# Performance work log

Hardware: AMD Instinct MI355X
Metric: run time of the kernel (lower is better)

## Reference

```python
import jax, jax.numpy as jnp
import numpy as np

B, T, E = 2, 2048, 2048
H, D = 16, 128
KVH = H // 2
THETA = 10000.0

def make_rope(dim, seq_len, theta):
    inv_freqs = 1.0 / (theta ** (jnp.arange(0, dim, 2, dtype=jnp.float32) / dim))
    positions = jnp.arange(seq_len, dtype=jnp.float32)
    freqs = positions[:, None] * inv_freqs[None, :]  # (T, D/2)
    return jax.lax.complex(jnp.cos(freqs), jnp.sin(freqs))

def apply_rope(x, rope):
    # x: (B, h, T, D), rope: (T, D/2) complex
    xr = x.astype(jnp.float32).reshape(*x.shape[:-1], -1, 2)
    xc = jax.lax.complex(xr[..., 0], xr[..., 1])
    out = xc * rope[None, None, :, :]
    return jnp.stack([jnp.real(out), jnp.imag(out)], axis=-1).reshape(x.shape).astype(x.dtype)

def setup_inputs() -> dict:
    key = jax.random.key(0)
    ks = jax.random.split(key, 5)
    x = jax.random.normal(ks[0], (B, T, E), dtype=jnp.float32)
    mask = jnp.tril(jnp.ones((T, T), dtype=jnp.int32))[None, None]  # causal (1,1,T,T)
    s = 0.02
    wq = jax.random.normal(ks[1], (E, H * D), dtype=jnp.float32) * s
    wk = jax.random.normal(ks[2], (E, KVH * D), dtype=jnp.float32) * s
    wv = jax.random.normal(ks[3], (E, KVH * D), dtype=jnp.float32) * s
    wo = jax.random.normal(ks[4], (H * D, E), dtype=jnp.float32) * s
    return {"x": x, "mask": mask, "wq": wq, "wk": wk, "wv": wv, "wo": wo}

def reference(x, mask, wq, wk, wv, wo):
    rope = make_rope(D, T, THETA)
    q = (x @ wq).reshape(B, T, H, D).transpose(0, 2, 1, 3)      # (B,H,T,D)
    k = (x @ wk).reshape(B, T, KVH, D).transpose(0, 2, 1, 3)    # (B,KVH,T,D)
    v = (x @ wv).reshape(B, T, KVH, D).transpose(0, 2, 1, 3)
    q = apply_rope(q, rope)
    k = apply_rope(k, rope)
    # GQA: repeat kv heads to match query heads
    k = jnp.repeat(k, H // KVH, axis=1)
    v = jnp.repeat(v, H // KVH, axis=1)
    scale = D ** -0.5
    attn = jnp.einsum('bhqd,bhkd->bhqk', q, k) * scale
    attn = jnp.where(mask == 0, -jnp.inf, attn)
    attn = jax.nn.softmax(attn, axis=-1)
    attn = jnp.where(jnp.isnan(attn), 0.0, attn)
    out = jnp.einsum('bhqk,bhkd->bhqd', attn, v)
    out = out.transpose(0, 2, 1, 3).reshape(B, T, H * D)
    return out @ wo
```

## Files before the change

### kernel.cpp

```cpp
#include <hip/hip_runtime.h>
#include <math.h>

#define Bb   2
#define Tt   2048
#define Ee   2048
#define Hh   16
#define KVHh 8
#define Dd   128
#define Mm   (Bb*Tt)

typedef unsigned short u16;
typedef __bf16 bf16x8 __attribute__((ext_vector_type(8)));
typedef float  f32x4  __attribute__((ext_vector_type(4)));

__device__ __forceinline__ u16 f2b(float f) {
    union { float f; unsigned u; } v; v.f = f;
    unsigned r = v.u + 0x7fffu + ((v.u >> 16) & 1u);
    return (u16)(r >> 16);
}
__device__ __forceinline__ u16 f2b_fast(float f) {
    union { float f; unsigned u; } v; v.f = f;
    return (u16)((v.u + 0x8000u) >> 16);
}
__device__ __forceinline__ float b2f(u16 h) {
    union { float f; unsigned u; } v; v.u = ((unsigned)h) << 16;
    return v.f;
}

__device__ __forceinline__ void gl_lds16(const u16* g, u16* l) {
    __builtin_amdgcn_global_load_lds(
        (const __attribute__((address_space(1))) void*)g,
        (__attribute__((address_space(3))) void*)l,
        16, 0, 0);
}

__global__ void cast_x_kernel(const float* __restrict__ x, u16* __restrict__ xb, int n4) {
    int i = blockIdx.x * blockDim.x + threadIdx.x;
    if (i >= n4) return;
    float4 f = ((const float4*)x)[i];
    unsigned lo = (unsigned)f2b(f.x) | ((unsigned)f2b(f.y) << 16);
    unsigned hi = (unsigned)f2b(f.z) | ((unsigned)f2b(f.w) << 16);
    ((uint2*)xb)[i] = make_uint2(lo, hi);
}

__global__ void addf4_kernel(float* __restrict__ o, const float* __restrict__ a, int n4) {
    int i = blockIdx.x * blockDim.x + threadIdx.x;
    if (i >= n4) return;
    float4 x = ((const float4*)o)[i];
    float4 y = ((const float4*)a)[i];
    x.x += y.x; x.y += y.y; x.z += y.z; x.w += y.w;
    ((float4*)o)[i] = x;
}

__global__ void transpose_cast4_kernel(const float* __restrict__ wq, const float* __restrict__ wk,
                                       const float* __restrict__ wv, const float* __restrict__ wo,
                                       u16* __restrict__ btqkv, u16* __restrict__ bto) {
    __shared__ float tile[32][33];
    int job = blockIdx.z;
    const float* W; u16* Bt; int C;
    if (job == 0)      { W = wq; Bt = btqkv;                      C = 2048; }
    else if (job == 1) { W = wk; Bt = btqkv + (size_t)2048 * Ee;  C = 1024; }
    else if (job == 2) { W = wv; Bt = btqkv + (size_t)3072 * Ee;  C = 1024; }
    else               { W = wo; Bt = bto;                        C = 2048; }
    int c0 = blockIdx.x * 32, r0 = blockIdx.y * 32;
    if (c0 >= C) return;
    int x = threadIdx.x, y = threadIdx.y;
    for (int j = y; j < 32; j += 8)
        tile[j][x] = W[(size_t)(r0 + j) * C + c0 + x];
    __syncthreads();
    for (int j = y; j < 32; j += 8)
        Bt[(size_t)(c0 + j) * 2048 + r0 + x] = f2b(tile[x][j]);
}

__global__ void transpose_v_kernel(const u16* __restrict__ v, u16* __restrict__ vt) {
    __shared__ u16 tile[32][34];
    int x = threadIdx.x, y = threadIdx.y;
    int c0 = blockIdx.x * 32;
    int r0 = blockIdx.y * 32;
    int bk = blockIdx.z;
    for (int j = y; j < 32; j += 8)
        tile[j][x] = v[((size_t)bk * Tt + r0 + j) * Dd + c0 + x];
    __syncthreads();
    for (int j = y; j < 32; j += 8)
        vt[((size_t)bk * Dd + c0 + j) * Tt + r0 + x] = tile[x][j];
}

__global__ void rope_kernel(u16* __restrict__ q, u16* __restrict__ k) {
    const int QP = Bb * Hh * Tt * (Dd / 2);
    const int KP = Bb * KVHh * Tt * (Dd / 2);
    int idx = blockIdx.x * blockDim.x + threadIdx.x;
    if (idx >= QP + KP) return;
    u16* ptr; int p;
    if (idx < QP) { ptr = q; p = idx; } else { ptr = k; p = idx - QP; }
    int d2 = p & 63;
    int row = p >> 6;
    int t = row & (Tt - 1);
    float ex = (float)(2 * d2) * (1.0f / 128.0f);
    float inv = expf(-ex * 9.210340371976184f);
    float fr = (float)t * inv;
    float c = cosf(fr), s = sinf(fr);
    size_t e0 = (size_t)row * Dd + 2 * d2;
    unsigned pair = *(const unsigned*)(ptr + e0);
    float x0 = b2f((u16)(pair & 0xffff));
    float x1 = b2f((u16)(pair >> 16));
    float o0 = x0 * c - x1 * s;
    float o1 = x0 * s + x1 * c;
    *(unsigned*)(ptr + e0) = (unsigned)f2b(o0) | ((unsigned)f2b(o1) << 16);
}

__global__ __launch_bounds__(512, 2) void gemm8_kernel(
    const u16* __restrict__ A0, const u16* __restrict__ Bt0,
    int Ndim, int Kdim, int Kstride, int mode,
    u16* __restrict__ qo, u16* __restrict__ ko, u16* __restrict__ vo,
    float* __restrict__ fo, float* __restrict__ fo2)
{
    __shared__ u16 sm[2][2][256 * 64];
    const int tid = threadIdx.x;
    const int lane = tid & 63, w = tid >> 6;
    const int quad = lane >> 4, l15 = lane & 15;
    const int bn = blockIdx.x, bm = blockIdx.y, kz = blockIdx.z;
    const u16* A  = A0  + (size_t)kz * Kdim;
    const u16* Bt = Bt0 + (size_t)kz * Kdim;
    const int wm = (w >> 2) * 128, wn = (w & 3) * 64;
    const int rowA0 = bm * 256, rowB0 = bn * 256;

    const int srow = lane >> 3;
    const int scolsw = (((lane & 7) ^ srow) << 3);
    const int wa = w & 3, wb = w >> 2;
    const int cAlo = (wm >> 3) + 2 * wa;
    const int cAhi = (wm >> 3) + 8 + 2 * wa;
    const int cBlo = (wn >> 3) + 2 * wb;
    const int cBhi = (wn >> 3) + 4 + 2 * wb;

    const int col0 = ((quad ^ (l15 & 7)) << 3);
    const int col1 = (((4 | quad) ^ (l15 & 7)) << 3);

    f32x4 acc[8][4];
#pragma unroll
    for (int i = 0; i < 8; i++)
#pragma unroll
        for (int j = 0; j < 4; j++) acc[i][j] = (f32x4){0.f, 0.f, 0.f, 0.f};

#define STAGE_PAIR(G, Grow0, ldsb, cb, kk) do { \
    gl_lds16((G) + (size_t)((Grow0) + (cb) * 8 + srow) * Kstride + (kk) + scolsw, \
             (ldsb) + (cb) * 512); \
    gl_lds16((G) + (size_t)((Grow0) + (cb) * 8 + 8 + srow) * Kstride + (kk) + scolsw, \
             (ldsb) + (cb) * 512 + 512); \
} while (0)

    STAGE_PAIR(A,  rowA0, &sm[0][0][0], cAlo, 0);
    STAGE_PAIR(Bt, rowB0, &sm[0][1][0], cBlo, 0);
    STAGE_PAIR(Bt, rowB0, &sm[0][1][0], cBhi, 0);
    STAGE_PAIR(A,  rowA0, &sm[0][0][0], cAhi, 0);
    asm volatile("s_waitcnt vmcnt(4)" ::: "memory");
    __builtin_amdgcn_s_barrier();
    __builtin_amdgcn_sched_barrier(0);

    bf16x8 a4[4][2], bA[2][2], bB[2][2];
    const int NT = Kdim >> 6;

    for (int t = 0; t < NT; ++t) {
        u16* As = &sm[t & 1][0][0];
        u16* Bs = &sm[t & 1][1][0];
        u16* An = &sm[(t + 1) & 1][0][0];
        u16* Bn = &sm[(t + 1) & 1][1][0];
        const int kk = (t + 1) << 6;
        const bool st = (t + 1 < NT);

#pragma unroll
        for (int i = 0; i < 4; i++) {
            const u16* p = As + (wm + i * 16 + l15) * 64;
            a4[i][0] = *(const bf16x8*)(p + col0);
            a4[i][1] = *(const bf16x8*)(p + col1);
        }
#pragma unroll
        for (int j = 0; j < 2; j++) {
            const u16* p = Bs + (wn + j * 16 + l15) * 64;
            bA[j][0] = *(const bf16x8*)(p + col0);
            bA[j][1] = *(const bf16x8*)(p + col1);
        }
        if (st) STAGE_PAIR(A, rowA0, An, cAlo, kk);
        __builtin_amdgcn_sched_barrier(0);
        __builtin_amdgcn_s_barrier();
        __builtin_amdgcn_sched_barrier(0);
        __builtin_amdgcn_s_setprio(1);
#pragma unroll
        for (int kc = 0; kc < 2; kc++)
#pragma unroll
            for (int i = 0; i < 4; i++)
#pragma unroll
                for (int j = 0; j < 2; j++)
                    acc[i][j] = __builtin_amdgcn_mfma_f32_16x16x32_bf16(a4[i][kc], bA[j][kc], acc[i][j], 0, 0, 0);
        __builtin_amdgcn_s_setprio(0);
        __builtin_amdgcn_sched_barrier(0);
        if (st) { asm volatile("s_waitcnt vmcnt(4)" ::: "memory"); }
        else    { asm volatile("s_waitcnt vmcnt(2)" ::: "memory"); }
        __builtin_amdgcn_s_barrier();
        __builtin_amdgcn_sched_barrier(0);

#pragma unroll
        for (int j = 0; j < 2; j++) {
            const u16* p = Bs + (wn + 32 + j * 16 + l15) * 64;
            bB[j][0] = *(const bf16x8*)(p + col0);
            bB[j][1] = *(const bf16x8*)(p + col1);
        }
        if (st) STAGE_PAIR(Bt, rowB0, Bn, cBlo, kk);
        __builtin_amdgcn_sched_barrier(0);
        __builtin_amdgcn_s_barrier();
        __builtin_amdgcn_sched_barrier(0);
        __builtin_amdgcn_s_setprio(1);
#pragma unroll
        for (int kc = 0; kc < 2; kc++)
#pragma unroll
            for (int i = 0; i < 4; i++)
#pragma unroll
                for (int j = 0; j < 2; j++)
                    acc[i][j + 2] = __builtin_amdgcn_mfma_f32_16x16x32_bf16(a4[i][kc], bB[j][kc], acc[i][j + 2], 0, 0, 0);
        __builtin_amdgcn_s_setprio(0);
        __builtin_amdgcn_sched_barrier(0);
        if (st) { asm volatile("s_waitcnt vmcnt(4)" ::: "memory"); }
        else    { asm volatile("s_waitcnt vmcnt(0)" ::: "memory"); }
        __builtin_amdgcn_s_barrier();
        __builtin_amdgcn_sched_barrier(0);

#pragma unroll
        for (int i = 0; i < 4; i++) {
            const u16* p = As + (wm + 64 + i * 16 + l15) * 64;
            a4[i][0] = *(const bf16x8*)(p + col0);
            a4[i][1] = *(const bf16x8*)(p + col1);
        }
        if (st) STAGE_PAIR(Bt, rowB0, Bn, cBhi, kk);
        __builtin_amdgcn_sched_barrier(0);
        __builtin_amdgcn_s_barrier();
        __builtin_amdgcn_sched_barrier(0);
        __builtin_amdgcn_s_setprio(1);
#pragma unroll
        for (int kc = 0; kc < 2; kc++)
#pragma unroll
            for (int i = 0; i < 4; i++)
#pragma unroll
                for (int j = 0; j < 2; j++)
                    acc[i + 4][j] = __builtin_amdgcn_mfma_f32_16x16x32_bf16(a4[i][kc], bA[j][kc], acc[i + 4][j], 0, 0, 0);
        __builtin_amdgcn_s_setprio(0);
        __builtin_amdgcn_sched_barrier(0);
        if (st) { asm volatile("s_waitcnt vmcnt(4)" ::: "memory"); }
        __builtin_amdgcn_s_barrier();
        __builtin_amdgcn_sched_barrier(0);

        if (st) STAGE_PAIR(A, rowA0, An, cAhi, kk);
        __builtin_amdgcn_sched_barrier(0);
        __builtin_amdgcn_s_barrier();
        __builtin_amdgcn_sched_barrier(0);
        __builtin_amdgcn_s_setprio(1);
#pragma unroll
        for (int kc = 0; kc < 2; kc++)
#pragma unroll
            for (int i = 0; i < 4; i++)
#pragma unroll
                for (int j = 0; j < 2; j++)
                    acc[i + 4][j + 2] = __builtin_amdgcn_mfma_f32_16x16x32_bf16(a4[i][kc], bB[j][kc], acc[i + 4][j + 2], 0, 0, 0);
        __builtin_amdgcn_s_setprio(0);
        __builtin_amdgcn_sched_barrier(0);
        if (st) { asm volatile("s_waitcnt vmcnt(4)" ::: "memory"); }
        __builtin_amdgcn_s_barrier();
        __builtin_amdgcn_sched_barrier(0);
    }
#undef STAGE_PAIR

    float* ft = kz ? fo2 : fo;
#pragma unroll
    for (int i = 0; i < 8; i++)
#pragma unroll
        for (int j = 0; j < 4; j++)
#pragma unroll
            for (int r = 0; r < 4; r++) {
                int m = rowA0 + wm + i * 16 + quad * 4 + r;
                int n = rowB0 + wn + j * 16 + l15;
                float val = acc[i][j][r];
                if (mode == 0) {
                    int b = m >> 11, tq = m & (Tt - 1);
                    if (n < 2048) {
                        int h = n >> 7, d = n & 127;
                        qo[(((size_t)(b * Hh + h)) * Tt + tq) * Dd + d] = f2b(val);
                    } else if (n < 3072) {
                        int h = (n - 2048) >> 7, d = n & 127;
                        ko[(((size_t)(b * KVHh + h)) * Tt + tq) * Dd + d] = f2b(val);
                    } else {
                        int h = (n - 3072) >> 7, d = n & 127;
                        vo[(((size_t)(b * KVHh + h)) * Tt + tq) * Dd + d] = f2b(val);
                    }
                } else {
                    ft[(size_t)m * Ndim + n] = val;
                }
            }
}

#define LDKV 136
#define LDVT 72
#define LDP  72
#define GRPU (64*LDKV + 128*LDVT + 128*LDP)

__global__ __launch_bounds__(512) void flash_kernel(
    const u16* __restrict__ q, const u16* __restrict__ k, const u16* __restrict__ vt,
    u16* __restrict__ attn)
{
    __shared__ u16 S[2 * GRPU];

    int tid = threadIdx.x;
    int grp = tid >> 8;
    int gtid = tid & 255;
    int lane = tid & 63, w4 = gtid >> 6;
    int quad = lane >> 4, l15 = lane & 15;
    int pr = blockIdx.x;
    int bh = blockIdx.y;
    int b = bh >> 4, h = bh & 15;
    int kvh = h >> 1;
    const u16* qbase = q + (size_t)bh * Tt * Dd;
    const u16* kbase = k + ((size_t)(b * KVHh + kvh)) * Tt * Dd;
    const u16* vtbase = vt + ((size_t)(b * KVHh + kvh)) * Dd * Tt;

    u16* Ksh  = S + grp * GRPU;
    u16* Vtsh = Ksh + 64 * LDKV;
    u16* Psh  = Vtsh + 128 * LDVT;
    u16* P0 = Psh + (2 * w4) * 16 * LDP;
    u16* P1 = Psh + (2 * w4 + 1) * 16 * LDP;
    u16* KA = S;
    u16* VA = S + 64 * LDKV;

    const float sc2 = 0.08838834764831845f * 1.4426950408889634f;
    const int qt_h = 15 - pr;
    const int light_nkt = 2 * (pr + 1);

    const int krow = gtid >> 4, kcol = (gtid & 15) * 8;
    const int vrow = gtid >> 3, vcol = (gtid & 7) * 8;

    int qt = grp ? pr : qt_h;
    int row0 = qt * 128 + w4 * 32;

    bf16x8 qf0[4], qf1[4];
#define LOAD_QF() do { \
    const u16* qr0 = qbase + (size_t)(row0 + l15) * Dd + quad * 8; \
    const u16* qr1 = qbase + (size_t)(row0 + 16 + l15) * Dd + quad * 8; \
    _Pragma("unroll") \
    for (int c = 0; c < 4; c++) { \
        qf0[c] = *(const bf16x8*)(qr0 + c * 32); \
        qf1[c] = *(const bf16x8*)(qr1 + c * 32); \
    } \
} while (0)
    LOAD_QF();

    f32x4 o0[8], o1[8];
#pragma unroll
    for (int i = 0; i < 8; i++) { o0[i] = (f32x4){0.f,0.f,0.f,0.f}; o1[i] = (f32x4){0.f,0.f,0.f,0.f}; }
    float l0[4] = {0.f,0.f,0.f,0.f}, l1[4] = {0.f,0.f,0.f,0.f};

    for (int it = 0; it < 17; it++) {
        if (grp == 1 && it == light_nkt) {
            float linv0[4], linv1[4];
#pragma unroll
            for (int r = 0; r < 4; r++) {
                float a = l0[r];
                a += __shfl_xor(a, 1); a += __shfl_xor(a, 2);
                a += __shfl_xor(a, 4); a += __shfl_xor(a, 8);
                linv0[r] = 1.0f / a;
                float c2 = l1[r];
                c2 += __shfl_xor(c2, 1); c2 += __shfl_xor(c2, 2);
                c2 += __shfl_xor(c2, 4); c2 += __shfl_xor(c2, 8);
                linv1[r] = 1.0f / c2;
            }
#pragma unroll
            for (int di = 0; di < 8; di++)
#pragma unroll
                for (int r = 0; r < 4; r++) {
                    int ta = row0 + quad * 4 + r;
                    int tb = row0 + 16 + quad * 4 + r;
                    size_t ma = (size_t)b * Tt + ta;
                    size_t mb = (size_t)b * Tt + tb;
                    attn[ma * (Hh * Dd) + h * Dd + di * 16 + l15] = f2b(o0[di][r] * linv0[r]);
                    attn[mb * (Hh * Dd) + h * Dd + di * 16 + l15] = f2b(o1[di][r] * linv1[r]);
                }
#pragma unroll
            for (int i = 0; i < 8; i++) { o0[i] = (f32x4){0.f,0.f,0.f,0.f}; o1[i] = (f32x4){0.f,0.f,0.f,0.f}; }
#pragma unroll
            for (int r = 0; r < 4; r++) { l0[r] = 0.f; l1[r] = 0.f; }
            qt = qt_h; row0 = qt * 128 + w4 * 32;
            LOAD_QF();
        }
        const int kt = (grp == 0) ? it : (it < light_nkt ? it : 17 + (it - light_nkt));
        const bool shareA = (grp == 1) && (it < light_nkt);
        const u16* Kr = shareA ? KA : Ksh;
        const u16* Vr = shareA ? VA : Vtsh;

        if (!shareA) {
#pragma unroll
            for (int j = 0; j < 4; j++) {
                int chunk = j * 256 + gtid;
                int rk = chunk >> 4, ck = chunk & 15;
                uint4 dk = *(const uint4*)(kbase + (size_t)(kt * 64 + rk) * Dd + ck * 8);
                *(uint4*)(Ksh + rk * LDKV + ck * 8) = dk;
                int rv = chunk >> 3, cv = chunk & 7;
                uint4 dv = *(const uint4*)(vtbase + (size_t)rv * Tt + kt * 64 + cv * 8);
                *(uint4*)(Vtsh + rv * LDVT + cv * 8) = dv;
            }
        }
        __syncthreads();

        bool skip = (kt * 64) > (row0 + 31);
        if (!skip) {
            f32x4 s0[4], s1[4];
#pragma unroll
            for (int ni = 0; ni < 4; ni++) { s0[ni] = (f32x4){0.f,0.f,0.f,0.f}; s1[ni] = (f32x4){0.f,0.f,0.f,0.f}; }
#pragma unroll
            for (int c = 0; c < 4; c++)
#pragma unroll
                for (int ni = 0; ni < 4; ni++) {
                    bf16x8 kf = *(const bf16x8*)(Kr + (ni * 16 + l15) * LDKV + c * 32 + quad * 8);
                    s0[ni] = __builtin_amdgcn_mfma_f32_16x16x32_bf16(qf0[c], kf, s0[ni], 0, 0, 0);
                    s1[ni] = __builtin_amdgcn_mfma_f32_16x16x32_bf16(qf1[c], kf, s1[ni], 0, 0, 0);
                }

            if (kt * 64 + 63 > row0) {
#pragma unroll
                for (int ni = 0; ni < 4; ni++)
#pragma unroll
                    for (int r = 0; r < 4; r++) {
                        int kcolm = kt * 64 + ni * 16 + l15;
                        int qa = row0 + quad * 4 + r;
                        int qb2 = row0 + 16 + quad * 4 + r;
                        if (kcolm > qa)  s0[ni][r] = -__builtin_inff();
                        if (kcolm > qb2) s1[ni][r] = -__builtin_inff();
                    }
            }

#pragma unroll
            for (int ni = 0; ni < 4; ni++)
#pragma unroll
                for (int r = 0; r < 4; r++) {
                    float p0 = exp2f(s0[ni][r] * sc2);
                    l0[r] += p0;
                    P0[(quad * 4 + r) * LDP + ni * 16 + l15] = f2b_fast(p0);
                    float p1 = exp2f(s1[ni][r] * sc2);
                    l1[r] += p1;
                    P1[(quad * 4 + r) * LDP + ni * 16 + l15] = f2b_fast(p1);
                }
        }
        __syncthreads();

        if (!skip) {
#pragma unroll
            for (int c = 0; c < 2; c++) {
                bf16x8 pf0 = *(const bf16x8*)(P0 + l15 * LDP + c * 32 + quad * 8);
                bf16x8 pf1 = *(const bf16x8*)(P1 + l15 * LDP + c * 32 + quad * 8);
#pragma unroll
                for (int di = 0; di < 8; di++) {
                    bf16x8 vf = *(const bf16x8*)(Vr + (di * 16 + l15) * LDVT + c * 32 + quad * 8);
                    o0[di] = __builtin_amdgcn_mfma_f32_16x16x32_bf16(pf0, vf, o0[di], 0, 0, 0);
                    o1[di] = __builtin_amdgcn_mfma_f32_16x16x32_bf16(pf1, vf, o1[di], 0, 0, 0);
                }
            }
        }
        __syncthreads();
    }

    float* Obuf = (float*)S;
    float* Lbuf = (float*)((char*)S + 128 * 132 * 4);
    if (grp == 1) {
        float ls0[4], ls1[4];
#pragma unroll
        for (int r = 0; r < 4; r++) {
            float a = l0[r];
            a += __shfl_xor(a, 1); a += __shfl_xor(a, 2);
            a += __shfl_xor(a, 4); a += __shfl_xor(a, 8);
            ls0[r] = a;
            float c2 = l1[r];
            c2 += __shfl_xor(c2, 1); c2 += __shfl_xor(c2, 2);
            c2 += __shfl_xor(c2, 4); c2 += __shfl_xor(c2, 8);
            ls1[r] = c2;
        }
#pragma unroll
        for (int di = 0; di < 8; di++)
#pragma unroll
            for (int r = 0; r < 4; r++) {
                Obuf[(w4 * 32 + quad * 4 + r) * 132 + di * 16 + l15] = o0[di][r];
                Obuf[(w4 * 32 + 16 + quad * 4 + r) * 132 + di * 16 + l15] = o1[di][r];
            }
        if (l15 == 0)
#pragma unroll
            for (int r = 0; r < 4; r++) {
                Lbuf[w4 * 32 + quad * 4 + r] = ls0[r];
                Lbuf[w4 * 32 + 16 + quad * 4 + r] = ls1[r];
            }
    }
    __syncthreads();
    if (grp == 0) {
        float linv0[4], linv1[4];
#pragma unroll
        for (int r = 0; r < 4; r++) {
            float a = l0[r];
            a += __shfl_xor(a, 1); a += __shfl_xor(a, 2);
            a += __shfl_xor(a, 4); a += __shfl_xor(a, 8);
            linv0[r] = 1.0f / (a + Lbuf[w4 * 32 + quad * 4 + r]);
            float c2 = l1[r];
            c2 += __shfl_xor(c2, 1); c2 += __shfl_xor(c2, 2);
            c2 += __shfl_xor(c2, 4); c2 += __shfl_xor(c2, 8);
            linv1[r] = 1.0f / (c2 + Lbuf[w4 * 32 + 16 + quad * 4 + r]);
        }
#pragma unroll
        for (int di = 0; di < 8; di++)
#pragma unroll
            for (int r = 0; r < 4; r++) {
                float v0 = o0[di][r] + Obuf[(w4 * 32 + quad * 4 + r) * 132 + di * 16 + l15];
                float v1 = o1[di][r] + Obuf[(w4 * 32 + 16 + quad * 4 + r) * 132 + di * 16 + l15];
                int ta = row0 + quad * 4 + r;
                int tb = row0 + 16 + quad * 4 + r;
                size_t ma = (size_t)b * Tt + ta;
                size_t mb = (size_t)b * Tt + tb;
                attn[ma * (Hh * Dd) + h * Dd + di * 16 + l15] = f2b(v0 * linv0[r]);
                attn[mb * (Hh * Dd) + h * Dd + di * 16 + l15] = f2b(v1 * linv1[r]);
            }
    }
#undef LOAD_QF
}

extern "C" void kernel_launch(void* const* d_in, const int* in_sizes, int n_in,
                              void* d_out, int out_size, void* d_ws, size_t ws_size,
                              hipStream_t stream) {
    const float* x  = (const float*)d_in[0];
    const float* wq = (const float*)d_in[2];
    const float* wk = (const float*)d_in[3];
    const float* wv = (const float*)d_in[4];
    const float* wo = (const float*)d_in[5];
    float* out = (float*)d_out;

    char* ws = (char*)d_ws;
    u16* xb    = (u16*)ws; ws += (size_t)Mm * Ee * 2;
    u16* btqkv = (u16*)ws; ws += (size_t)4096 * Ee * 2;
    u16* bto   = (u16*)ws; ws += (size_t)Ee * (Hh * Dd) * 2;
    u16* qb    = (u16*)ws; ws += (size_t)Bb * Hh * Tt * Dd * 2;
    u16* kb    = (u16*)ws; ws += (size_t)Bb * KVHh * Tt * Dd * 2;
    u16* vb    = (u16*)ws; ws += (size_t)Bb * KVHh * Tt * Dd * 2;
    u16* vtb   = (u16*)ws; ws += (size_t)Bb * KVHh * Dd * Tt * 2;
    u16* attn  = (u16*)ws; ws += (size_t)Mm * (Hh * Dd) * 2;

    float* fo2 = (float*)qb;

    cast_x_kernel<<<(Mm * Ee / 4 + 255) / 256, 256, 0, stream>>>(x, xb, Mm * Ee / 4);

    transpose_cast4_kernel<<<dim3(64, 64, 4), dim3(32, 8), 0, stream>>>(wq, wk, wv, wo, btqkv, bto);

    gemm8_kernel<<<dim3(16, 16, 1), 512, 0, stream>>>(xb, btqkv, 4096, Ee, Ee, 0,
                                                      qb, kb, vb, nullptr, nullptr);

    {
        int total = Bb * Hh * Tt * 64 + Bb * KVHh * Tt * 64;
        rope_kernel<<<(total + 255) / 256, 256, 0, stream>>>(qb, kb);
    }

    transpose_v_kernel<<<dim3(Dd / 32, Tt / 32, Bb * KVHh), dim3(32, 8), 0, stream>>>(vb, vtb);

    flash_kernel<<<dim3(Tt / 256, Bb * Hh), 512, 0, stream>>>(qb, kb, vtb, attn);

    gemm8_kernel<<<dim3(8, 16, 2), 512, 0, stream>>>(attn, bto, 2048, (Hh * Dd) / 2, Hh * Dd, 1,
                                                     nullptr, nullptr, nullptr, out, fo2);
    addf4_kernel<<<(Mm * Ee / 4 + 255) / 256, 256, 0, stream>>>(out, fo2, Mm * Ee / 4);
}
```

Before: 361.9 us.

## Restructure GEMM LDS pipeline with split A registers and early B prefetch

The GEMM main loop now keeps separate register sets for the low and high A halves. It loads the B fragments for the next iteration ahead of the last MFMA block, and merges the first two compute phases so one barrier round is removed. The vmcnt waits are tightened to match the new staging order. In the attention kernel, a __syncthreads between writing the P tile and the PV MFMA is removed, which relies on each wave reading only the P rows it wrote itself. The aim is fewer barriers and better overlap of LDS reads with MFMA, at the cost of more registers and possible LDS race hazards.

New measurement: 358.7 us. Within noise of the previous version (-0.9%).

```diff
diff --git a/kernel.cpp b/kernel.cpp
--- a/kernel.cpp
+++ b/kernel.cpp
@@ -152,12 +152,19 @@
     STAGE_PAIR(Bt, rowB0, &sm[0][1][0], cBlo, 0);
     STAGE_PAIR(Bt, rowB0, &sm[0][1][0], cBhi, 0);
     STAGE_PAIR(A,  rowA0, &sm[0][0][0], cAhi, 0);
-    asm volatile("s_waitcnt vmcnt(4)" ::: "memory");
+    asm volatile("s_waitcnt vmcnt(2)" ::: "memory");
     __builtin_amdgcn_s_barrier();
     __builtin_amdgcn_sched_barrier(0);
 
-    bf16x8 a4[4][2], bA[2][2], bB[2][2];
+    bf16x8 a4lo[4][2], a4hi[4][2], bA[2][2], bB[2][2];
     const int NT = Kdim >> 6;
+
+#pragma unroll
+    for (int j = 0; j < 2; j++) {
+        const u16* p = &sm[0][1][0] + (wn + j * 16 + l15) * 64;
+        bA[j][0] = *(const bf16x8*)(p + col0);
+        bA[j][1] = *(const bf16x8*)(p + col1);
+    }
 
     for (int t = 0; t < NT; ++t) {
         u16* As = &sm[t & 1][0][0];
@@ -170,40 +177,35 @@
 #pragma unroll
         for (int i = 0; i < 4; i++) {
             const u16* p = As + (wm + i * 16 + l15) * 64;
-            a4[i][0] = *(const bf16x8*)(p + col0);
-            a4[i][1] = *(const bf16x8*)(p + col1);
-        }
-#pragma unroll
-        for (int j = 0; j < 2; j++) {
-            const u16* p = Bs + (wn + j * 16 + l15) * 64;
-            bA[j][0] = *(const bf16x8*)(p + col0);
-            bA[j][1] = *(const bf16x8*)(p + col1);
+            a4lo[i][0] = *(const bf16x8*)(p + col0);
+            a4lo[i][1] = *(const bf16x8*)(p + col1);
         }
         if (st) STAGE_PAIR(A, rowA0, An, cAlo, kk);
         __builtin_amdgcn_sched_barrier(0);
         __builtin_amdgcn_s_barrier();
         __builtin_amdgcn_sched_barrier(0);
-        __builtin_amdgcn_s_setprio(1);
-#pragma unroll
-        for (int kc = 0; kc < 2; kc++)
-#pragma unroll
-            for (int i = 0; i < 4; i++)
-#pragma unroll
-                for (int j = 0; j < 2; j++)
-                    acc[i][j] = __builtin_amdgcn_mfma_f32_16x16x32_bf16(a4[i][kc], bA[j][kc], acc[i][j], 0, 0, 0);
-        __builtin_amdgcn_s_setprio(0);
-        __builtin_amdgcn_sched_barrier(0);
-        if (st) { asm volatile("s_waitcnt vmcnt(4)" ::: "memory"); }
-        else    { asm volatile("s_waitcnt vmcnt(2)" ::: "memory"); }
-        __builtin_amdgcn_s_barrier();
-        __builtin_amdgcn_sched_barrier(0);
-
 #pragma unroll
         for (int j = 0; j < 2; j++) {
             const u16* p = Bs + (wn + 32 + j * 16 + l15) * 64;
             bB[j][0] = *(const bf16x8*)(p + col0);
             bB[j][1] = *(const bf16x8*)(p + col1);
         }
+        __builtin_amdgcn_sched_barrier(0);
+        __builtin_amdgcn_s_setprio(1);
+#pragma unroll
+        for (int kc = 0; kc < 2; kc++)
+#pragma unroll
+            for (int i = 0; i < 4; i++)
+#pragma unroll
+                for (int j = 0; j < 2; j++)
+                    acc[i][j] = __builtin_amdgcn_mfma_f32_16x16x32_bf16(a4lo[i][kc], bA[j][kc], acc[i][j], 0, 0, 0);
+        __builtin_amdgcn_s_setprio(0);
+        __builtin_amdgcn_sched_barrier(0);
+        if (st) { asm volatile("s_waitcnt vmcnt(2)" ::: "memory"); }
+        else    { asm volatile("s_waitcnt vmcnt(0)" ::: "memory"); }
+        __builtin_amdgcn_s_barrier();
+        __builtin_amdgcn_sched_barrier(0);
+
         if (st) STAGE_PAIR(Bt, rowB0, Bn, cBlo, kk);
         __builtin_amdgcn_sched_barrier(0);
         __builtin_amdgcn_s_barrier();
@@ -215,19 +217,18 @@
             for (int i = 0; i < 4; i++)
 #pragma unroll
                 for (int j = 0; j < 2; j++)
-                    acc[i][j + 2] = __builtin_amdgcn_mfma_f32_16x16x32_bf16(a4[i][kc], bB[j][kc], acc[i][j + 2], 0, 0, 0);
+                    acc[i][j + 2] = __builtin_amdgcn_mfma_f32_16x16x32_bf16(a4lo[i][kc], bB[j][kc], acc[i][j + 2], 0, 0, 0);
         __builtin_amdgcn_s_setprio(0);
         __builtin_amdgcn_sched_barrier(0);
-        if (st) { asm volatile("s_waitcnt vmcnt(4)" ::: "memory"); }
-        else    { asm volatile("s_waitcnt vmcnt(0)" ::: "memory"); }
+        if (st) { asm volatile("s_waitcnt vmcnt(2)" ::: "memory"); }
         __builtin_amdgcn_s_barrier();
         __builtin_amdgcn_sched_barrier(0);
 
 #pragma unroll
         for (int i = 0; i < 4; i++) {
             const u16* p = As + (wm + 64 + i * 16 + l15) * 64;
-            a4[i][0] = *(const bf16x8*)(p + col0);
-            a4[i][1] = *(const bf16x8*)(p + col1);
+            a4hi[i][0] = *(const bf16x8*)(p + col0);
+            a4hi[i][1] = *(const bf16x8*)(p + col1);
         }
         if (st) STAGE_PAIR(Bt, rowB0, Bn, cBhi, kk);
         __builtin_amdgcn_sched_barrier(0);
@@ -240,10 +241,10 @@
             for (int i = 0; i < 4; i++)
 #pragma unroll
                 for (int j = 0; j < 2; j++)
-                    acc[i + 4][j] = __builtin_amdgcn_mfma_f32_16x16x32_bf16(a4[i][kc], bA[j][kc], acc[i + 4][j], 0, 0, 0);
+                    acc[i + 4][j] = __builtin_amdgcn_mfma_f32_16x16x32_bf16(a4hi[i][kc], bA[j][kc], acc[i + 4][j], 0, 0, 0);
         __builtin_amdgcn_s_setprio(0);
         __builtin_amdgcn_sched_barrier(0);
-        if (st) { asm volatile("s_waitcnt vmcnt(4)" ::: "memory"); }
+        if (st) { asm volatile("s_waitcnt vmcnt(2)" ::: "memory"); }
         __builtin_amdgcn_s_barrier();
         __builtin_amdgcn_sched_barrier(0);
 
@@ -251,6 +252,15 @@
         __builtin_amdgcn_sched_barrier(0);
         __builtin_amdgcn_s_barrier();
         __builtin_amdgcn_sched_barrier(0);
+        if (st) {
+#pragma unroll
+            for (int j = 0; j < 2; j++) {
+                const u16* p = Bn + (wn + j * 16 + l15) * 64;
+                bA[j][0] = *(const bf16x8*)(p + col0);
+                bA[j][1] = *(const bf16x8*)(p + col1);
+            }
+        }
+        __builtin_amdgcn_sched_barrier(0);
         __builtin_amdgcn_s_setprio(1);
 #pragma unroll
         for (int kc = 0; kc < 2; kc++)
@@ -258,10 +268,10 @@
             for (int i = 0; i < 4; i++)
 #pragma unroll
                 for (int j = 0; j < 2; j++)
-                    acc[i + 4][j + 2] = __builtin_amdgcn_mfma_f32_16x16x32_bf16(a4[i][kc], bB[j][kc], acc[i + 4][j + 2], 0, 0, 0);
+                    acc[i + 4][j + 2] = __builtin_amdgcn_mfma_f32_16x16x32_bf16(a4hi[i][kc], bB[j][kc], acc[i + 4][j + 2], 0, 0, 0);
         __builtin_amdgcn_s_setprio(0);
         __builtin_amdgcn_sched_barrier(0);
-        if (st) { asm volatile("s_waitcnt vmcnt(4)" ::: "memory"); }
+        if (st) { asm volatile("s_waitcnt vmcnt(2)" ::: "memory"); }
         __builtin_amdgcn_s_barrier();
         __builtin_amdgcn_sched_barrier(0);
     }
@@ -443,10 +453,8 @@
                     l1[r] += p1;
                     P1[(quad * 4 + r) * LDP + ni * 16 + l15] = f2b_fast(p1);
                 }
-        }
-        __syncthreads();
-
-        if (!skip) {
+
+
 #pragma unroll
             for (int c = 0; c < 2; c++) {
                 bf16x8 pf0 = *(const bf16x8*)(P0 + l15 * LDP + c * 32 + quad * 8);
```

## Replace split-K output projection with 128x256-tile GEMM and drop add kernel

Applied to the files above, without the earlier changes.

The output projection previously ran as a split-K (2-way) 256x256-tile GEMM writing two fp32 partial buffers, followed by a separate elementwise add kernel. A new GEMM kernel uses 128x256 tiles over the full K, launching 256 blocks directly into the output, which removes the partial-sum write, reread and extra launch. The flash kernel also drops a __syncthreads between writing P to LDS and the PV MFMA, which cuts a barrier but risks a race if P rows are read across waves.

New measurement: 346.2 us. 1.05x faster.

```diff
diff --git a/kernel.cpp b/kernel.cpp
--- a/kernel.cpp
+++ b/kernel.cpp
@@ -41,15 +41,6 @@
     unsigned lo = (unsigned)f2b(f.x) | ((unsigned)f2b(f.y) << 16);
     unsigned hi = (unsigned)f2b(f.z) | ((unsigned)f2b(f.w) << 16);
     ((uint2*)xb)[i] = make_uint2(lo, hi);
-}
-
-__global__ void addf4_kernel(float* __restrict__ o, const float* __restrict__ a, int n4) {
-    int i = blockIdx.x * blockDim.x + threadIdx.x;
-    if (i >= n4) return;
-    float4 x = ((const float4*)o)[i];
-    float4 y = ((const float4*)a)[i];
-    x.x += y.x; x.y += y.y; x.z += y.z; x.w += y.w;
-    ((float4*)o)[i] = x;
 }
 
 __global__ void transpose_cast4_kernel(const float* __restrict__ wq, const float* __restrict__ wk,
@@ -112,15 +103,15 @@
     const u16* __restrict__ A0, const u16* __restrict__ Bt0,
     int Ndim, int Kdim, int Kstride, int mode,
     u16* __restrict__ qo, u16* __restrict__ ko, u16* __restrict__ vo,
-    float* __restrict__ fo, float* __restrict__ fo2)
+    float* __restrict__ fo)
 {
     __shared__ u16 sm[2][2][256 * 64];
     const int tid = threadIdx.x;
     const int lane = tid & 63, w = tid >> 6;
     const int quad = lane >> 4, l15 = lane & 15;
-    const int bn = blockIdx.x, bm = blockIdx.y, kz = blockIdx.z;
-    const u16* A  = A0  + (size_t)kz * Kdim;
-    const u16* Bt = Bt0 + (size_t)kz * Kdim;
+    const int bn = blockIdx.x, bm = blockIdx.y;
+    const u16* A  = A0;
+    const u16* Bt = Bt0;
     const int wm = (w >> 2) * 128, wn = (w & 3) * 64;
     const int rowA0 = bm * 256, rowB0 = bn * 256;
 
@@ -267,7 +258,6 @@
     }
 #undef STAGE_PAIR
 
-    float* ft = kz ? fo2 : fo;
 #pragma unroll
     for (int i = 0; i < 8; i++)
 #pragma unroll
@@ -290,8 +280,166 @@
                         vo[(((size_t)(b * KVHh + h)) * Tt + tq) * Dd + d] = f2b(val);
                     }
                 } else {
-                    ft[(size_t)m * Ndim + n] = val;
+                    fo[(size_t)m * Ndim + n] = val;
                 }
+            }
+}
+
+__global__ __launch_bounds__(512, 2) void gemm8n_kernel(
+    const u16* __restrict__ A, const u16* __restrict__ Bt,
+    int Ndim, int Kdim,
+    float* __restrict__ fo)
+{
+    __shared__ u16 sm[2][384 * 64];
+    const int tid = threadIdx.x;
+    const int lane = tid & 63, w = tid >> 6;
+    const int quad = lane >> 4, l15 = lane & 15;
+    const int bn = blockIdx.x, bm = blockIdx.y;
+    const int wm = (w >> 2) * 64, wn = (w & 3) * 64;
+    const int rowA0 = bm * 128, rowB0 = bn * 256;
+
+    const int srow = lane >> 3;
+    const int scolsw = (((lane & 7) ^ srow) << 3);
+    const int cA = 2 * w;
+    const int cBlo = ((w & 3) * 8) + 2 * (w >> 2);
+    const int cBhi = cBlo + 4;
+
+    const int col0 = ((quad ^ (l15 & 7)) << 3);
+    const int col1 = (((4 | quad) ^ (l15 & 7)) << 3);
+
+    f32x4 acc[4][4];
+#pragma unroll
+    for (int i = 0; i < 4; i++)
+#pragma unroll
+        for (int j = 0; j < 4; j++) acc[i][j] = (f32x4){0.f, 0.f, 0.f, 0.f};
+
+#define STAGE_PAIR(G, Grow0, ldsb, cb, kk) do { \
+    gl_lds16((G) + (size_t)((Grow0) + (cb) * 8 + srow) * Kdim + (kk) + scolsw, \
+             (ldsb) + (cb) * 512); \
+    gl_lds16((G) + (size_t)((Grow0) + (cb) * 8 + 8 + srow) * Kdim + (kk) + scolsw, \
+             (ldsb) + (cb) * 512 + 512); \
+} while (0)
+
+    STAGE_PAIR(A,  rowA0, &sm[0][0],        cA, 0);
+    STAGE_PAIR(Bt, rowB0, &sm[0][128 * 64], cBlo, 0);
+    STAGE_PAIR(Bt, rowB0, &sm[0][128 * 64], cBhi, 0);
+    asm volatile("s_waitcnt vmcnt(2)" ::: "memory");
+    __builtin_amdgcn_s_barrier();
+    __builtin_amdgcn_sched_barrier(0);
+
+    bf16x8 alo[2][2], ahi[2][2], bA[2][2], bB[2][2];
+    const int NT = Kdim >> 6;
+
+    for (int t = 0; t < NT; ++t) {
+        u16* As = &sm[t & 1][0];
+        u16* Bs = &sm[t & 1][128 * 64];
+        u16* An = &sm[(t + 1) & 1][0];
+        u16* Bn = &sm[(t + 1) & 1][128 * 64];
+        const int kk = (t + 1) << 6;
+        const bool st = (t + 1 < NT);
+
+#pragma unroll
+        for (int i = 0; i < 2; i++) {
+            const u16* p = As + (wm + i * 16 + l15) * 64;
+            alo[i][0] = *(const bf16x8*)(p + col0);
+            alo[i][1] = *(const bf16x8*)(p + col1);
+        }
+#pragma unroll
+        for (int j = 0; j < 2; j++) {
+            const u16* p = Bs + (wn + j * 16 + l15) * 64;
+            bA[j][0] = *(const bf16x8*)(p + col0);
+            bA[j][1] = *(const bf16x8*)(p + col1);
+        }
+        if (st) STAGE_PAIR(A, rowA0, An, cA, kk);
+        __builtin_amdgcn_sched_barrier(0);
+        __builtin_amdgcn_s_barrier();
+        __builtin_amdgcn_sched_barrier(0);
+        __builtin_amdgcn_s_setprio(1);
+#pragma unroll
+        for (int kc = 0; kc < 2; kc++)
+#pragma unroll
+            for (int i = 0; i < 2; i++)
+#pragma unroll
+                for (int j = 0; j < 2; j++)
+                    acc[i][j] = __builtin_amdgcn_mfma_f32_16x16x32_bf16(alo[i][kc], bA[j][kc], acc[i][j], 0, 0, 0);
+        __builtin_amdgcn_s_setprio(0);
+        __builtin_amdgcn_sched_barrier(0);
+        if (st) { asm volatile("s_waitcnt vmcnt(2)" ::: "memory"); }
+        else    { asm volatile("s_waitcnt vmcnt(0)" ::: "memory"); }
+        __builtin_amdgcn_s_barrier();
+        __builtin_amdgcn_sched_barrier(0);
+
+#pragma unroll
+        for (int j = 0; j < 2; j++) {
+            const u16* p = Bs + (wn + 32 + j * 16 + l15) * 64;
+            bB[j][0] = *(const bf16x8*)(p + col0);
+            bB[j][1] = *(const bf16x8*)(p + col1);
+        }
+        if (st) STAGE_PAIR(Bt, rowB0, Bn, cBlo, kk);
+        __builtin_amdgcn_sched_barrier(0);
+        __builtin_amdgcn_s_barrier();
+        __builtin_amdgcn_sched_barrier(0);
+        __builtin_amdgcn_s_setprio(1);
+#pragma unroll
+        for (int kc = 0; kc < 2; kc++)
+#pragma unroll
+            for (int i = 0; i < 2; i++)
+#pragma unroll
+                for (int j = 0; j < 2; j++)
+                    acc[i][j + 2] = __builtin_amdgcn_mfma_f32_16x16x32_bf16(alo[i][kc], bB[j][kc], acc[i][j + 2], 0, 0, 0);
+        __builtin_amdgcn_s_setprio(0);
+        __builtin_amdgcn_sched_barrier(0);
+        __builtin_amdgcn_s_barrier();
+        __builtin_amdgcn_sched_barrier(0);
+
+#pragma unroll
+        for (int i = 0; i < 2; i++) {
+            const u16* p = As + (wm + 32 + i * 16 + l15) * 64;
+            ahi[i][0] = *(const bf16x8*)(p + col0);
+            ahi[i][1] = *(const bf16x8*)(p + col1);
+        }
+        if (st) STAGE_PAIR(Bt, rowB0, Bn, cBhi, kk);
+        __builtin_amdgcn_sched_barrier(0);
+        __builtin_amdgcn_s_barrier();
+        __builtin_amdgcn_sched_barrier(0);
+        __builtin_amdgcn_s_setprio(1);
+#pragma unroll
+        for (int kc = 0; kc < 2; kc++)
+#pragma unroll
+            for (int i = 0; i < 2; i++)
+#pragma unroll
+                for (int j = 0; j < 2; j++)
+                    acc[i + 2][j] = __builtin_amdgcn_mfma_f32_16x16x32_bf16(ahi[i][kc], bA[j][kc], acc[i + 2][j], 0, 0, 0);
+        __builtin_amdgcn_s_setprio(0);
+        __builtin_amdgcn_sched_barrier(0);
+        __builtin_amdgcn_s_barrier();
+        __builtin_amdgcn_sched_barrier(0);
+
+        __builtin_amdgcn_s_setprio(1);
+#pragma unroll
+        for (int kc = 0; kc < 2; kc++)
+#pragma unroll
+            for (int i = 0; i < 2; i++)
+#pragma unroll
+                for (int j = 0; j < 2; j++)
+                    acc[i + 2][j + 2] = __builtin_amdgcn_mfma_f32_16x16x32_bf16(ahi[i][kc], bB[j][kc], acc[i + 2][j + 2], 0, 0, 0);
+        __builtin_amdgcn_s_setprio(0);
+        __builtin_amdgcn_sched_barrier(0);
+        if (st) { asm volatile("s_waitcnt vmcnt(2)" ::: "memory"); }
+        __builtin_amdgcn_s_barrier();
+        __builtin_amdgcn_sched_barrier(0);
+    }
+#undef STAGE_PAIR
+
+#pragma unroll
+    for (int i = 0; i < 4; i++)
+#pragma unroll
+        for (int j = 0; j < 4; j++)
+#pragma unroll
+            for (int r = 0; r < 4; r++) {
+                int m = rowA0 + wm + i * 16 + quad * 4 + r;
+                int n = rowB0 + wn + j * 16 + l15;
+                fo[(size_t)m * Ndim + n] = acc[i][j][r];
             }
 }
 
@@ -443,10 +591,8 @@
                     l1[r] += p1;
                     P1[(quad * 4 + r) * LDP + ni * 16 + l15] = f2b_fast(p1);
                 }
-        }
-        __syncthreads();
-
-        if (!skip) {
+
+
 #pragma unroll
             for (int c = 0; c < 2; c++) {
                 bf16x8 pf0 = *(const bf16x8*)(P0 + l15 * LDP + c * 32 + quad * 8);
@@ -542,14 +688,12 @@
     u16* vtb   = (u16*)ws; ws += (size_t)Bb * KVHh * Dd * Tt * 2;
     u16* attn  = (u16*)ws; ws += (size_t)Mm * (Hh * Dd) * 2;
 
-    float* fo2 = (float*)qb;
-
     cast_x_kernel<<<(Mm * Ee / 4 + 255) / 256, 256, 0, stream>>>(x, xb, Mm * Ee / 4);
 
     transpose_cast4_kernel<<<dim3(64, 64, 4), dim3(32, 8), 0, stream>>>(wq, wk, wv, wo, btqkv, bto);
 
-    gemm8_kernel<<<dim3(16, 16, 1), 512, 0, stream>>>(xb, btqkv, 4096, Ee, Ee, 0,
-                                                      qb, kb, vb, nullptr, nullptr);
+    gemm8_kernel<<<dim3(16, 16), 512, 0, stream>>>(xb, btqkv, 4096, Ee, Ee, 0,
+                                                   qb, kb, vb, nullptr);
 
     {
         int total = Bb * Hh * Tt * 64 + Bb * KVHh * Tt * 64;
@@ -560,7 +704,5 @@
 
     flash_kernel<<<dim3(Tt / 256, Bb * Hh), 512, 0, stream>>>(qb, kb, vtb, attn);
 
-    gemm8_kernel<<<dim3(8, 16, 2), 512, 0, stream>>>(attn, bto, 2048, (Hh * Dd) / 2, Hh * Dd, 1,
-                                                     nullptr, nullptr, nullptr, out, fo2);
-    addf4_kernel<<<(Mm * Ee / 4 + 255) / 256, 256, 0, stream>>>(out, fo2, Mm * Ee / 4);
-}
+    gemm8n_kernel<<<dim3(8, 32), 512, 0, stream>>>(attn, bto, 2048, Hh * Dd, out);
+}
```
